# Kernel optimization log

Hardware: AMD Instinct MI355X
Metric: run time of the kernel (lower is better)

Reference implementation:

```python
import jax, jax.numpy as jnp
import numpy as np

B, S, P, HID, HQ, HKV, D, MAXP = 8, 4, 4096, 4096, 32, 8, 128, 8192


def setup_inputs() -> dict:
    key = jax.random.key(0)
    ks = jax.random.split(key, 8)
    # rotary tables (Llama-style: freqs duplicated across halves)
    inv_freq = 1.0 / (10000.0 ** (jnp.arange(0, D // 2, dtype=jnp.float32) / (D // 2)))
    t = jnp.arange(MAXP, dtype=jnp.float32)
    emb = jnp.concatenate([jnp.outer(t, inv_freq)] * 2, axis=-1)  # [MAXP, D]
    w = 0.02
    return {
        "x": jax.random.normal(ks[0], (B, S, HID), dtype=jnp.float32),
        "wq": w * jax.random.normal(ks[1], (HID, HQ * D), dtype=jnp.float32),
        "wk": w * jax.random.normal(ks[2], (HID, HKV * D), dtype=jnp.float32),
        "wv": w * jax.random.normal(ks[3], (HID, HKV * D), dtype=jnp.float32),
        "wo": w * jax.random.normal(ks[4], (HQ * D, HID), dtype=jnp.float32),
        "cos": jnp.cos(emb),
        "sin": jnp.sin(emb),
        "k_cache": jax.random.normal(ks[5], (B, P, HKV, D), dtype=jnp.float32),
        "v_cache": jax.random.normal(ks[6], (B, P, HKV, D), dtype=jnp.float32),
        "past_len": P,
    }


def _rope(x, c, s):
    # x: [B,S,H,D]; c,s: [1,S,1,D] -- half-rotation RoPE
    half = x.shape[-1] // 2
    x1, x2 = x[..., :half], x[..., half:]
    return x * c + jnp.concatenate([-x2, x1], axis=-1) * s


def reference(x, wq, wk, wv, wo, cos, sin, k_cache, v_cache, past_len):
    b, s, _ = x.shape
    hq, hkv, d = HQ, HKV, D
    q = (x @ wq).reshape(b, s, hq, d)
    k = (x @ wk).reshape(b, s, hkv, d)
    v = (x @ wv).reshape(b, s, hkv, d)

    pos = past_len + jnp.arange(s)                     # new-token positions
    c = cos[pos][None, :, None, :]
    sn = sin[pos][None, :, None, :]
    q = _rope(q, c, sn)
    k = _rope(k, c, sn)

    # append new kv to cache
    k_all = jnp.concatenate([k_cache, k], axis=1)      # [B,T,HKV,D]
    v_all = jnp.concatenate([v_cache, v], axis=1)
    t_len = k_all.shape[1]

    group = hq // hkv
    qg = q.reshape(b, s, hkv, group, d)
    scores = jnp.einsum('bskgd,btkd->bkgst', qg, k_all) / jnp.sqrt(jnp.asarray(d, x.dtype))

    # causal: query at position past_len+i attends to key positions <= past_len+i
    key_pos = jnp.arange(t_len)
    mask = pos[:, None] >= key_pos[None, :]            # [S,T]
    scores = jnp.where(mask[None, None, None], scores, jnp.asarray(-1e30, scores.dtype))
    attn = jax.nn.softmax(scores, axis=-1)

    out = jnp.einsum('bkgst,btkd->bskgd', attn, v_all).reshape(b, s, hq * d)
    return out @ wo
```

## Files before the change

kernel.cpp:

```cpp
#include <hip/hip_runtime.h>
#include <math.h>

#define NB 8
#define NS 4
#define NP 4096
#define HID 4096
#define NHQ 32
#define NHKV 8
#define ND 128
#define NGROUP 4
#define NBS 32
#define NQI 16
#define NCHUNK 17
#define TCHUNK 256
#define QKV_COLS 6144
#define LOG2E 1.4426950408889634f

__global__ __launch_bounds__(256) void prep_xT(const float* __restrict__ x,
                                               float* __restrict__ xT) {
  int n = blockIdx.x * 256 + threadIdx.x;
  int r = n >> 12;
  int k = n & 4095;
  xT[k * NBS + r] = x[n];
}

__global__ __launch_bounds__(256) void rope_kernel(
    const float* __restrict__ qb, const float* __restrict__ kb,
    const float* __restrict__ cosp, const float* __restrict__ sinp,
    const int* __restrict__ past_len, float* __restrict__ q_t,
    float* __restrict__ k_new) {
  int n = blockIdx.x * 256 + threadIdx.x;
  int pl = past_len[0];
  if (n < NBS * HID) {
    int r = n >> 12;
    int hd = n & 4095;
    int h = hd >> 7, d = hd & 127;
    int b = r >> 2, s = r & 3;
    int pos = pl + s;
    float c = cosp[pos * ND + d], sn = sinp[pos * ND + d];
    float v = qb[n];
    float other = (d < 64) ? -qb[n + 64] : qb[n - 64];
    float rv = fmaf(v, c, other * sn);
    int kv = h >> 2, g = h & 3;
    q_t[(((b * NHKV + kv) * ND + d) * NQI) + g * NS + s] = rv;
  } else {
    n -= NBS * HID;
    int r = n >> 10;
    int hd = n & 1023;
    int kv = hd >> 7, d = hd & 127;
    int b = r >> 2, s = r & 3;
    int pos = pl + s;
    float c = cosp[pos * ND + d], sn = sinp[pos * ND + d];
    float v = kb[n];
    float other = (d < 64) ? -kb[n + 64] : kb[n - 64];
    k_new[((b * NHKV + kv) * NS + s) * ND + d] = fmaf(v, c, other * sn);
  }
}

template <int KSLICE>
__global__ __launch_bounds__(256) void gemm_part(
    const float* __restrict__ A_T, const float* __restrict__ wq,
    const float* __restrict__ wk, const float* __restrict__ wv,
    const float* __restrict__ wo, float* __restrict__ P, int mode) {
  __shared__ __align__(16) float lds[8192];
  int cb = blockIdx.x, kb = blockIdx.y;
  int ncols = mode ? 4096 : QKV_COLS;
  int col0 = cb * 128;
  const float* W;
  int ld, wcol;
  if (mode) {
    W = wo; ld = 4096; wcol = col0;
  } else if (col0 < 4096) {
    W = wq; ld = 4096; wcol = col0;
  } else if (col0 < 5120) {
    W = wk; ld = 1024; wcol = col0 - 4096;
  } else {
    W = wv; ld = 1024; wcol = col0 - 5120;
  }
  int tid = threadIdx.x;
  int lane = tid & 63;
  int wid = __builtin_amdgcn_readfirstlane(tid >> 6);
  int l32 = lane & 31;
  int mh = lane >> 5;
  int kblk = kb * KSLICE;
  constexpr int KW = KSLICE / 4;
  int k0 = wid * KW;
  const float* wp = W + (size_t)(kblk + k0) * ld + wcol + l32 * 4;

  float4 wb[8];
#pragma unroll
  for (int u = 0; u < 8; u++) wb[u] = *(const float4*)(wp + (size_t)u * ld);

  {
    const float4* src = (const float4*)(A_T + (size_t)kblk * NBS);
    float4* dst = (float4*)lds;
#pragma unroll
    for (int p = 0; p < KSLICE / 32; p++)
      dst[p * 256 + tid] = src[p * 256 + tid];
  }
  __syncthreads();

  float acc[64];
#pragma unroll
  for (int v = 0; v < 64; v++) acc[v] = 0.f;

  const float* xp = lds + (size_t)k0 * NBS + mh * 16;

  auto body = [&](int kk, float4 w) {
    const float* xr = xp + (size_t)kk * NBS;
    float4 xa = *(const float4*)(xr);
    float4 xb = *(const float4*)(xr + 4);
    float4 xc = *(const float4*)(xr + 8);
    float4 xd = *(const float4*)(xr + 12);
    float xm[16] = {xa.x, xa.y, xa.z, xa.w, xb.x, xb.y, xb.z, xb.w,
                    xc.x, xc.y, xc.z, xc.w, xd.x, xd.y, xd.z, xd.w};
#pragma unroll
    for (int m = 0; m < 16; m++) {
      acc[4 * m + 0] = fmaf(xm[m], w.x, acc[4 * m + 0]);
      acc[4 * m + 1] = fmaf(xm[m], w.y, acc[4 * m + 1]);
      acc[4 * m + 2] = fmaf(xm[m], w.z, acc[4 * m + 2]);
      acc[4 * m + 3] = fmaf(xm[m], w.w, acc[4 * m + 3]);
    }
  };

#pragma unroll 8
  for (int kk = 0; kk < KW - 8; kk++) {
    float4 w = wb[kk & 7];
    wb[kk & 7] = *(const float4*)(wp + (size_t)(kk + 8) * ld);
    body(kk, w);
  }
#pragma unroll
  for (int kk = KW - 8; kk < KW; kk++) {
    float4 w = wb[kk & 7];
    body(kk, w);
  }

  __syncthreads();
  if (wid >= 2) {
#pragma unroll
    for (int v = 0; v < 64; v++) lds[(wid - 2) * 4096 + v * 64 + lane] = acc[v];
  }
  __syncthreads();
  if (wid < 2) {
#pragma unroll
    for (int v = 0; v < 64; v++) acc[v] += lds[wid * 4096 + v * 64 + lane];
  }
  __syncthreads();
  if (wid == 1) {
#pragma unroll
    for (int v = 0; v < 64; v++) lds[v * 64 + lane] = acc[v];
  }
  __syncthreads();
  if (wid == 0) {
#pragma unroll
    for (int v = 0; v < 64; v++) acc[v] += lds[v * 64 + lane];
#pragma unroll
    for (int m = 0; m < 16; m++) {
      float4 st = make_float4(acc[4 * m], acc[4 * m + 1], acc[4 * m + 2],
                              acc[4 * m + 3]);
      *(float4*)(P + ((size_t)kb * NBS + mh * 16 + m) * ncols + col0 +
                 l32 * 4) = st;
    }
  }
}

template <int KS>
__global__ __launch_bounds__(256) void reduce_qkv(const float* __restrict__ P,
                                                  float* __restrict__ qb,
                                                  float* __restrict__ kbuf,
                                                  float* __restrict__ vbuf) {
  size_t idx = ((size_t)blockIdx.x * 256 + threadIdx.x) * 4;
  float4 s = make_float4(0.f, 0.f, 0.f, 0.f);
#pragma unroll
  for (int p = 0; p < KS; p++) {
    float4 v = *(const float4*)(P + (size_t)p * (NBS * QKV_COLS) + idx);
    s.x += v.x; s.y += v.y; s.z += v.z; s.w += v.w;
  }
  int r = (int)(idx / QKV_COLS);
  int col = (int)(idx % QKV_COLS);
  float* dst;
  if (col < 4096)
    dst = qb + (size_t)r * 4096 + col;
  else if (col < 5120)
    dst = kbuf + (size_t)r * 1024 + (col - 4096);
  else
    dst = vbuf + (size_t)r * 1024 + (col - 5120);
  *(float4*)dst = s;
}

template <int KS>
__global__ __launch_bounds__(256) void reduce_o(const float* __restrict__ P,
                                                float* __restrict__ outp) {
  size_t idx = ((size_t)blockIdx.x * 256 + threadIdx.x) * 4;
  float4 s = make_float4(0.f, 0.f, 0.f, 0.f);
#pragma unroll
  for (int p = 0; p < KS; p++) {
    float4 v = *(const float4*)(P + (size_t)p * (NBS * 4096) + idx);
    s.x += v.x; s.y += v.y; s.z += v.z; s.w += v.w;
  }
  *(float4*)(outp + idx) = s;
}

__global__ __launch_bounds__(256) void attn_kernel(
    const float* __restrict__ q_t, const float* __restrict__ k_cache,
    const float* __restrict__ v_cache, const float* __restrict__ k_new,
    const float* __restrict__ vbuf, float* __restrict__ part_o,
    float* __restrict__ part_m, float* __restrict__ part_l) {
  __shared__ __align__(16) float sbuf[NQI * TCHUNK];
  __shared__ float redm[NQI][4];
  __shared__ float redl[NQI][4];
  __shared__ float mfin[NQI];
  float* p_lds = sbuf;
  int bk = blockIdx.x;
  int chunk = blockIdx.y;
  int blk = bk * NCHUNK + chunk;
  int b = bk >> 3, kv = bk & 7;
  int tid = threadIdx.x;
  int lane = tid & 63;
  int wid = tid >> 6;
  bool last = (chunk == NCHUNK - 1);
  int tcount = last ? NS : TCHUNK;
  const float* qbase = q_t + (size_t)bk * (ND * NQI);

  int t_loc = tid;
  bool valid = t_loc < tcount;
  int t_eff = valid ? t_loc : 0;
  const float* kp =
      last ? (k_new + ((size_t)bk * NS + t_eff) * ND)
           : (k_cache +
              (((size_t)b * NP + chunk * TCHUNK + t_eff) * NHKV + kv) * ND);
  float s_acc[NQI];
#pragma unroll
  for (int i = 0; i < NQI; i++) s_acc[i] = 0.f;
#pragma unroll 8
  for (int d4 = 0; d4 < 32; ++d4) {
    float4 kvv = *(const float4*)(kp + d4 * 4);
    const float* qp = qbase + (d4 * 4) * NQI;
#pragma unroll
    for (int i = 0; i < NQI; i++) {
      float s = s_acc[i];
      s = fmaf(kvv.x, qp[i], s);
      s = fmaf(kvv.y, qp[NQI + i], s);
      s = fmaf(kvv.z, qp[2 * NQI + i], s);
      s = fmaf(kvv.w, qp[3 * NQI + i], s);
      s_acc[i] = s;
    }
  }
  const float scale = 0.08838834764831845f;
  float sc[NQI];
#pragma unroll
  for (int i = 0; i < NQI; i++) {
    float s = s_acc[i] * scale;
    if (!valid || (last && t_loc > (i & 3))) s = -__builtin_inff();
    sc[i] = s;
  }
#pragma unroll
  for (int i = 0; i < NQI; i++) {
    float m = sc[i];
#pragma unroll
    for (int off = 1; off < 64; off <<= 1) m = fmaxf(m, __shfl_xor(m, off, 64));
    if (lane == 0) redm[i][wid] = m;
  }
  __syncthreads();
  if (tid < NQI) {
    mfin[tid] = fmaxf(fmaxf(redm[tid][0], redm[tid][1]),
                      fmaxf(redm[tid][2], redm[tid][3]));
  }
  __syncthreads();
  float l_loc[NQI];
#pragma unroll
  for (int i = 0; i < NQI; i++) {
    float p = exp2f((sc[i] - mfin[i]) * LOG2E);
    p_lds[i * TCHUNK + t_loc] = p;
    l_loc[i] = p;
  }
#pragma unroll
  for (int i = 0; i < NQI; i++) {
    float l = l_loc[i];
#pragma unroll
    for (int off = 1; off < 64; off <<= 1) l += __shfl_xor(l, off, 64);
    if (lane == 0) redl[i][wid] = l;
  }
  __syncthreads();
  if (tid < NQI) {
    part_m[(size_t)blk * NQI + tid] = mfin[tid];
    part_l[(size_t)blk * NQI + tid] =
        redl[tid][0] + redl[tid][1] + redl[tid][2] + redl[tid][3];
  }

  int g = tid >> 5;
  int dq = (tid & 31) * 4;
  int tbeg = g * 32;
  int tnum = tcount - tbeg;
  tnum = tnum < 0 ? 0 : (tnum > 32 ? 32 : tnum);
  const float* vpb =
      last ? (vbuf + ((size_t)b * NS + tbeg) * (NHKV * ND) + kv * ND + dq)
           : (v_cache + ((size_t)b * NP + chunk * TCHUNK + tbeg) * (NHKV * ND) +
              kv * ND + dq);
  float o[NQI][4];
#pragma unroll
  for (int i = 0; i < NQI; i++) o[i][0] = o[i][1] = o[i][2] = o[i][3] = 0.f;
#pragma unroll 4
  for (int tt = 0; tt < tnum; ++tt) {
    float4 vv = *(const float4*)(vpb + (size_t)tt * (NHKV * ND));
    const float* pp = p_lds + (tbeg + tt);
#pragma unroll
    for (int i = 0; i < NQI; i++) {
      float p = pp[i * TCHUNK];
      o[i][0] = fmaf(p, vv.x, o[i][0]);
      o[i][1] = fmaf(p, vv.y, o[i][1]);
      o[i][2] = fmaf(p, vv.z, o[i][2]);
      o[i][3] = fmaf(p, vv.w, o[i][3]);
    }
  }
#pragma unroll
  for (int i = 0; i < NQI; i++) {
#pragma unroll
    for (int c = 0; c < 4; c++) o[i][c] += __shfl_xor(o[i][c], 32, 64);
  }
  __syncthreads();
  float* red = sbuf;
  if (wid >= 2 && lane < 32) {
#pragma unroll
    for (int i = 0; i < NQI; i++)
      *(float4*)(red + ((wid - 2) * NQI + i) * 128 + dq) =
          make_float4(o[i][0], o[i][1], o[i][2], o[i][3]);
  }
  __syncthreads();
  if (wid < 2 && lane < 32) {
#pragma unroll
    for (int i = 0; i < NQI; i++) {
      float4 r = *(const float4*)(red + (wid * NQI + i) * 128 + dq);
      o[i][0] += r.x; o[i][1] += r.y; o[i][2] += r.z; o[i][3] += r.w;
    }
  }
  __syncthreads();
  if (wid == 1 && lane < 32) {
#pragma unroll
    for (int i = 0; i < NQI; i++)
      *(float4*)(red + i * 128 + dq) =
          make_float4(o[i][0], o[i][1], o[i][2], o[i][3]);
  }
  __syncthreads();
  if (wid == 0 && lane < 32) {
    size_t obase = (size_t)blk * (NQI * ND);
#pragma unroll
    for (int i = 0; i < NQI; i++) {
      float4 r = *(const float4*)(red + i * 128 + dq);
      *(float4*)(part_o + obase + (size_t)i * ND + dq) =
          make_float4(o[i][0] + r.x, o[i][1] + r.y, o[i][2] + r.z,
                      o[i][3] + r.w);
    }
  }
}

__global__ __launch_bounds__(256) void combine_kernel(
    const float* __restrict__ part_o, const float* __restrict__ part_m,
    const float* __restrict__ part_l, float* __restrict__ attn_T) {
  int bk = blockIdx.x;
  int tid = threadIdx.x;
  int i = tid >> 4;
  int dh = (tid & 15) * 4 + blockIdx.y * 64;
  float M = -__builtin_inff();
#pragma unroll
  for (int c = 0; c < NCHUNK; c++)
    M = fmaxf(M, part_m[((size_t)bk * NCHUNK + c) * NQI + i]);
  float L = 0.f;
  float o0 = 0.f, o1 = 0.f, o2 = 0.f, o3 = 0.f;
#pragma unroll
  for (int c = 0; c < NCHUNK; c++) {
    size_t pc = (size_t)bk * NCHUNK + c;
    float mc = part_m[pc * NQI + i];
    float w = exp2f((mc - M) * LOG2E);
    L = fmaf(part_l[pc * NQI + i], w, L);
    float4 po = *(const float4*)(part_o + pc * (NQI * ND) + (size_t)i * ND + dh);
    o0 = fmaf(w, po.x, o0);
    o1 = fmaf(w, po.y, o1);
    o2 = fmaf(w, po.z, o2);
    o3 = fmaf(w, po.w, o3);
  }
  float inv = 1.0f / L;
  int b = bk >> 3, kv = bk & 7;
  int g = i >> 2, s = i & 3;
  int h = kv * NGROUP + g;
  int r = b * NS + s;
  attn_T[(size_t)(h * ND + dh + 0) * NBS + r] = o0 * inv;
  attn_T[(size_t)(h * ND + dh + 1) * NBS + r] = o1 * inv;
  attn_T[(size_t)(h * ND + dh + 2) * NBS + r] = o2 * inv;
  attn_T[(size_t)(h * ND + dh + 3) * NBS + r] = o3 * inv;
}

extern "C" void kernel_launch(void* const* d_in, const int* in_sizes, int n_in,
                              void* d_out, int out_size, void* d_ws,
                              size_t ws_size, hipStream_t stream) {
  const float* x = (const float*)d_in[0];
  const float* wq = (const float*)d_in[1];
  const float* wk = (const float*)d_in[2];
  const float* wv = (const float*)d_in[3];
  const float* wo = (const float*)d_in[4];
  const float* cosp = (const float*)d_in[5];
  const float* sinp = (const float*)d_in[6];
  const float* k_cache = (const float*)d_in[7];
  const float* v_cache = (const float*)d_in[8];
  const int* past_len = (const int*)d_in[9];
  float* out = (float*)d_out;

  float* ws = (float*)d_ws;
  float* xT = ws;
  float* qb = xT + 131072;
  float* kbuf = qb + 131072;
  float* vbuf = kbuf + 32768;
  float* q_t = vbuf + 32768;
  float* k_new = q_t + 131072;
  float* attn_T = k_new + 32768;
  float* R = attn_T + 131072;
  float* Pq = R;
  float* part_o = R;
  float* part_m = R + 2228224;
  float* part_l = part_m + 17408;
  float* Po = R;

  const size_t need32 = (size_t)(622592 + 32 * NBS * QKV_COLS) * sizeof(float);
  const bool big = ws_size >= need32;

  prep_xT<<<512, 256, 0, stream>>>(x, xT);
  if (big) {
    gemm_part<128><<<dim3(48, 32), 256, 0, stream>>>(xT, wq, wk, wv, wo, Pq, 0);
    reduce_qkv<32><<<192, 256, 0, stream>>>(Pq, qb, kbuf, vbuf);
  } else {
    gemm_part<256><<<dim3(48, 16), 256, 0, stream>>>(xT, wq, wk, wv, wo, Pq, 0);
    reduce_qkv<16><<<192, 256, 0, stream>>>(Pq, qb, kbuf, vbuf);
  }
  rope_kernel<<<640, 256, 0, stream>>>(qb, kbuf, cosp, sinp, past_len, q_t,
                                       k_new);
  attn_kernel<<<dim3(64, NCHUNK), 256, 0, stream>>>(
      q_t, k_cache, v_cache, k_new, vbuf, part_o, part_m, part_l);
  combine_kernel<<<dim3(64, 2), 256, 0, stream>>>(part_o, part_m, part_l,
                                                  attn_T);
  if (big) {
    gemm_part<128><<<dim3(32, 32), 256, 0, stream>>>(attn_T, wq, wk, wv, wo,
                                                     Po, 1);
    reduce_o<32><<<128, 256, 0, stream>>>(Po, out);
  } else {
    gemm_part<256><<<dim3(32, 16), 256, 0, stream>>>(attn_T, wq, wk, wv, wo,
                                                     Po, 1);
    reduce_o<16><<<128, 256, 0, stream>>>(Po, out);
  }
}
```

Before: 464.6 us.

## Split attention into smaller chunks with head-dim split QK and query-half PV

The attention kernel is templated on chunk size. With enough workspace it uses 128-token chunks, giving 33 chunks and twice as many blocks. For those chunks the QK dot product is split across two thread halves over the head dimension and combined through LDS. The PV stage now gives each thread 8 queries instead of 16 and stores probabilities transposed with padding, which cuts register pressure and allows a higher occupancy hint. This adds more partials for the combine kernel, whose chunk loop is now a runtime count, and some extra LDS syncs.

```diff
diff --git a/kernel.cpp b/kernel.cpp
--- a/kernel.cpp
+++ b/kernel.cpp
@@ -11,8 +11,6 @@
 #define NGROUP 4
 #define NBS 32
 #define NQI 16
-#define NCHUNK 17
-#define TCHUNK 256
 #define QKV_COLS 6144
 #define LOG2E 1.4426950408889634f
 
@@ -201,153 +199,178 @@
   *(float4*)(outp + idx) = s;
 }
 
-__global__ __launch_bounds__(256) void attn_kernel(
+template <int TCH>
+__global__ __launch_bounds__(256, 6) void attn_kernel(
     const float* __restrict__ q_t, const float* __restrict__ k_cache,
     const float* __restrict__ v_cache, const float* __restrict__ k_new,
     const float* __restrict__ vbuf, float* __restrict__ part_o,
-    float* __restrict__ part_m, float* __restrict__ part_l) {
-  __shared__ __align__(16) float sbuf[NQI * TCHUNK];
+    float* __restrict__ part_m, float* __restrict__ part_l, int nch) {
+  constexpr int BUFN = (TCH * 17 > 4096) ? TCH * 17 : 4096;
+  constexpr int NWS = (TCH == 128) ? 2 : 4;
+  constexpr int NF4 = (TCH == 128) ? 16 : 32;
+  constexpr int TPV = TCH / 4;
+  __shared__ __align__(16) float sbuf[BUFN];
   __shared__ float redm[NQI][4];
   __shared__ float redl[NQI][4];
   __shared__ float mfin[NQI];
-  float* p_lds = sbuf;
   int bk = blockIdx.x;
   int chunk = blockIdx.y;
-  int blk = bk * NCHUNK + chunk;
+  int blk = bk * nch + chunk;
   int b = bk >> 3, kv = bk & 7;
   int tid = threadIdx.x;
   int lane = tid & 63;
   int wid = tid >> 6;
-  bool last = (chunk == NCHUNK - 1);
-  int tcount = last ? NS : TCHUNK;
+  bool last = (chunk == nch - 1);
+  int tcount = last ? NS : TCH;
   const float* qbase = q_t + (size_t)bk * (ND * NQI);
 
-  int t_loc = tid;
-  bool valid = t_loc < tcount;
-  int t_eff = valid ? t_loc : 0;
+  int t_loc = tid & (TCH - 1);
+  int dh = tid / TCH;
+  bool tvalid = t_loc < tcount;
+  int t_eff = tvalid ? t_loc : 0;
   const float* kp =
       last ? (k_new + ((size_t)bk * NS + t_eff) * ND)
            : (k_cache +
-              (((size_t)b * NP + chunk * TCHUNK + t_eff) * NHKV + kv) * ND);
+              (((size_t)b * NP + chunk * TCH + t_eff) * NHKV + kv) * ND);
+  kp += dh * 64;
   float s_acc[NQI];
 #pragma unroll
   for (int i = 0; i < NQI; i++) s_acc[i] = 0.f;
-#pragma unroll 8
-  for (int d4 = 0; d4 < 32; ++d4) {
-    float4 kvv = *(const float4*)(kp + d4 * 4);
-    const float* qp = qbase + (d4 * 4) * NQI;
-#pragma unroll
-    for (int i = 0; i < NQI; i++) {
-      float s = s_acc[i];
-      s = fmaf(kvv.x, qp[i], s);
-      s = fmaf(kvv.y, qp[NQI + i], s);
-      s = fmaf(kvv.z, qp[2 * NQI + i], s);
-      s = fmaf(kvv.w, qp[3 * NQI + i], s);
-      s_acc[i] = s;
+#pragma unroll 4
+  for (int i = 0; i < NF4; ++i) {
+    float4 kvv = *(const float4*)(kp + i * 4);
+    const float* qp = qbase + (dh * 64 + i * 4) * NQI;
+#pragma unroll
+    for (int q = 0; q < NQI; q++) {
+      float s = s_acc[q];
+      s = fmaf(kvv.x, qp[q], s);
+      s = fmaf(kvv.y, qp[NQI + q], s);
+      s = fmaf(kvv.z, qp[2 * NQI + q], s);
+      s = fmaf(kvv.w, qp[3 * NQI + q], s);
+      s_acc[q] = s;
+    }
+  }
+  if (TCH == 128) {
+    if (dh == 1) {
+#pragma unroll
+      for (int q = 0; q < NQI; q++) sbuf[t_loc * 17 + q] = s_acc[q];
+    }
+    __syncthreads();
+    if (dh == 0) {
+#pragma unroll
+      for (int q = 0; q < NQI; q++) s_acc[q] += sbuf[t_loc * 17 + q];
     }
   }
   const float scale = 0.08838834764831845f;
   float sc[NQI];
 #pragma unroll
-  for (int i = 0; i < NQI; i++) {
-    float s = s_acc[i] * scale;
-    if (!valid || (last && t_loc > (i & 3))) s = -__builtin_inff();
-    sc[i] = s;
-  }
-#pragma unroll
-  for (int i = 0; i < NQI; i++) {
-    float m = sc[i];
+  for (int q = 0; q < NQI; q++) {
+    float s = s_acc[q] * scale;
+    if (dh != 0 || !tvalid || (last && t_loc > (q & 3)))
+      s = -__builtin_inff();
+    sc[q] = s;
+  }
+#pragma unroll
+  for (int q = 0; q < NQI; q++) {
+    float m = sc[q];
 #pragma unroll
     for (int off = 1; off < 64; off <<= 1) m = fmaxf(m, __shfl_xor(m, off, 64));
-    if (lane == 0) redm[i][wid] = m;
+    if (lane == 0 && wid < NWS) redm[q][wid] = m;
   }
   __syncthreads();
   if (tid < NQI) {
-    mfin[tid] = fmaxf(fmaxf(redm[tid][0], redm[tid][1]),
-                      fmaxf(redm[tid][2], redm[tid][3]));
+    float m = redm[tid][0];
+#pragma unroll
+    for (int w = 1; w < NWS; w++) m = fmaxf(m, redm[tid][w]);
+    mfin[tid] = m;
   }
   __syncthreads();
   float l_loc[NQI];
-#pragma unroll
-  for (int i = 0; i < NQI; i++) {
-    float p = exp2f((sc[i] - mfin[i]) * LOG2E);
-    p_lds[i * TCHUNK + t_loc] = p;
-    l_loc[i] = p;
-  }
-#pragma unroll
-  for (int i = 0; i < NQI; i++) {
-    float l = l_loc[i];
-#pragma unroll
-    for (int off = 1; off < 64; off <<= 1) l += __shfl_xor(l, off, 64);
-    if (lane == 0) redl[i][wid] = l;
+  if (dh == 0) {
+#pragma unroll
+    for (int q = 0; q < NQI; q++) {
+      float p = exp2f((sc[q] - mfin[q]) * LOG2E);
+      sbuf[t_loc * 17 + q] = p;
+      l_loc[q] = p;
+    }
+  } else {
+#pragma unroll
+    for (int q = 0; q < NQI; q++) l_loc[q] = 0.f;
+  }
+  if (wid < NWS) {
+#pragma unroll
+    for (int q = 0; q < NQI; q++) {
+      float l = l_loc[q];
+#pragma unroll
+      for (int off = 1; off < 64; off <<= 1) l += __shfl_xor(l, off, 64);
+      if (lane == 0) redl[q][wid] = l;
+    }
   }
   __syncthreads();
   if (tid < NQI) {
+    float l = redl[tid][0];
+#pragma unroll
+    for (int w = 1; w < NWS; w++) l += redl[tid][w];
     part_m[(size_t)blk * NQI + tid] = mfin[tid];
-    part_l[(size_t)blk * NQI + tid] =
-        redl[tid][0] + redl[tid][1] + redl[tid][2] + redl[tid][3];
+    part_l[(size_t)blk * NQI + tid] = l;
   }
 
   int g = tid >> 5;
+  int qh = g & 1;
+  int tq = g >> 1;
   int dq = (tid & 31) * 4;
-  int tbeg = g * 32;
+  int tbeg = tq * TPV;
   int tnum = tcount - tbeg;
-  tnum = tnum < 0 ? 0 : (tnum > 32 ? 32 : tnum);
+  tnum = tnum < 0 ? 0 : (tnum > TPV ? TPV : tnum);
   const float* vpb =
       last ? (vbuf + ((size_t)b * NS + tbeg) * (NHKV * ND) + kv * ND + dq)
-           : (v_cache + ((size_t)b * NP + chunk * TCHUNK + tbeg) * (NHKV * ND) +
+           : (v_cache + ((size_t)b * NP + chunk * TCH + tbeg) * (NHKV * ND) +
               kv * ND + dq);
-  float o[NQI][4];
-#pragma unroll
-  for (int i = 0; i < NQI; i++) o[i][0] = o[i][1] = o[i][2] = o[i][3] = 0.f;
+  float o[8][4];
+#pragma unroll
+  for (int i = 0; i < 8; i++) o[i][0] = o[i][1] = o[i][2] = o[i][3] = 0.f;
 #pragma unroll 4
   for (int tt = 0; tt < tnum; ++tt) {
     float4 vv = *(const float4*)(vpb + (size_t)tt * (NHKV * ND));
-    const float* pp = p_lds + (tbeg + tt);
-#pragma unroll
-    for (int i = 0; i < NQI; i++) {
-      float p = pp[i * TCHUNK];
+    const float* pp = sbuf + (tbeg + tt) * 17 + qh * 8;
+#pragma unroll
+    for (int i = 0; i < 8; i++) {
+      float p = pp[i];
       o[i][0] = fmaf(p, vv.x, o[i][0]);
       o[i][1] = fmaf(p, vv.y, o[i][1]);
       o[i][2] = fmaf(p, vv.z, o[i][2]);
       o[i][3] = fmaf(p, vv.w, o[i][3]);
     }
   }
-#pragma unroll
-  for (int i = 0; i < NQI; i++) {
-#pragma unroll
-    for (int c = 0; c < 4; c++) o[i][c] += __shfl_xor(o[i][c], 32, 64);
-  }
-  __syncthreads();
-  float* red = sbuf;
-  if (wid >= 2 && lane < 32) {
-#pragma unroll
-    for (int i = 0; i < NQI; i++)
-      *(float4*)(red + ((wid - 2) * NQI + i) * 128 + dq) =
+  __syncthreads();
+  if (wid >= 2) {
+#pragma unroll
+    for (int i = 0; i < 8; i++)
+      *(float4*)(sbuf + (wid - 2) * 2048 + i * 256 + lane * 4) =
           make_float4(o[i][0], o[i][1], o[i][2], o[i][3]);
   }
   __syncthreads();
-  if (wid < 2 && lane < 32) {
-#pragma unroll
-    for (int i = 0; i < NQI; i++) {
-      float4 r = *(const float4*)(red + (wid * NQI + i) * 128 + dq);
+  if (wid < 2) {
+#pragma unroll
+    for (int i = 0; i < 8; i++) {
+      float4 r = *(const float4*)(sbuf + wid * 2048 + i * 256 + lane * 4);
       o[i][0] += r.x; o[i][1] += r.y; o[i][2] += r.z; o[i][3] += r.w;
     }
   }
   __syncthreads();
-  if (wid == 1 && lane < 32) {
-#pragma unroll
-    for (int i = 0; i < NQI; i++)
-      *(float4*)(red + i * 128 + dq) =
+  if (wid == 1) {
+#pragma unroll
+    for (int i = 0; i < 8; i++)
+      *(float4*)(sbuf + i * 256 + lane * 4) =
           make_float4(o[i][0], o[i][1], o[i][2], o[i][3]);
   }
   __syncthreads();
-  if (wid == 0 && lane < 32) {
+  if (wid == 0) {
     size_t obase = (size_t)blk * (NQI * ND);
 #pragma unroll
-    for (int i = 0; i < NQI; i++) {
-      float4 r = *(const float4*)(red + i * 128 + dq);
-      *(float4*)(part_o + obase + (size_t)i * ND + dq) =
+    for (int i = 0; i < 8; i++) {
+      float4 r = *(const float4*)(sbuf + i * 256 + lane * 4);
+      *(float4*)(part_o + obase + (size_t)(qh * 8 + i) * ND + dq) =
           make_float4(o[i][0] + r.x, o[i][1] + r.y, o[i][2] + r.z,
                       o[i][3] + r.w);
     }
@@ -356,20 +379,18 @@
 
 __global__ __launch_bounds__(256) void combine_kernel(
     const float* __restrict__ part_o, const float* __restrict__ part_m,
-    const float* __restrict__ part_l, float* __restrict__ attn_T) {
+    const float* __restrict__ part_l, float* __restrict__ attn_T, int nch) {
   int bk = blockIdx.x;
   int tid = threadIdx.x;
   int i = tid >> 4;
   int dh = (tid & 15) * 4 + blockIdx.y * 64;
   float M = -__builtin_inff();
-#pragma unroll
-  for (int c = 0; c < NCHUNK; c++)
-    M = fmaxf(M, part_m[((size_t)bk * NCHUNK + c) * NQI + i]);
+  for (int c = 0; c < nch; c++)
+    M = fmaxf(M, part_m[((size_t)bk * nch + c) * NQI + i]);
   float L = 0.f;
   float o0 = 0.f, o1 = 0.f, o2 = 0.f, o3 = 0.f;
-#pragma unroll
-  for (int c = 0; c < NCHUNK; c++) {
-    size_t pc = (size_t)bk * NCHUNK + c;
+  for (int c = 0; c < nch; c++) {
+    size_t pc = (size_t)bk * nch + c;
     float mc = part_m[pc * NQI + i];
     float w = exp2f((mc - M) * LOG2E);
     L = fmaf(part_l[pc * NQI + i], w, L);
@@ -414,17 +435,24 @@
   float* k_new = q_t + 131072;
   float* attn_T = k_new + 32768;
   float* R = attn_T + 131072;
+
+  size_t ws_fl = ws_size / sizeof(float);
+  int ksplit, nch;
+  if (ws_fl >= (size_t)622592 + 6291456) {
+    ksplit = 32; nch = 33;
+  } else if (ws_fl >= (size_t)622592 + 4392960) {
+    ksplit = 16; nch = 33;
+  } else {
+    ksplit = 16; nch = 17;
+  }
   float* Pq = R;
   float* part_o = R;
-  float* part_m = R + 2228224;
-  float* part_l = part_m + 17408;
+  float* part_m = R + (size_t)64 * nch * 2048;
+  float* part_l = part_m + (size_t)64 * nch * 16;
   float* Po = R;
 
-  const size_t need32 = (size_t)(622592 + 32 * NBS * QKV_COLS) * sizeof(float);
-  const bool big = ws_size >= need32;
-
   prep_xT<<<512, 256, 0, stream>>>(x, xT);
-  if (big) {
+  if (ksplit == 32) {
     gemm_part<128><<<dim3(48, 32), 256, 0, stream>>>(xT, wq, wk, wv, wo, Pq, 0);
     reduce_qkv<32><<<192, 256, 0, stream>>>(Pq, qb, kbuf, vbuf);
   } else {
@@ -433,11 +461,16 @@
   }
   rope_kernel<<<640, 256, 0, stream>>>(qb, kbuf, cosp, sinp, past_len, q_t,
                                        k_new);
-  attn_kernel<<<dim3(64, NCHUNK), 256, 0, stream>>>(
-      q_t, k_cache, v_cache, k_new, vbuf, part_o, part_m, part_l);
+  if (nch == 33) {
+    attn_kernel<128><<<dim3(64, 33), 256, 0, stream>>>(
+        q_t, k_cache, v_cache, k_new, vbuf, part_o, part_m, part_l, 33);
+  } else {
+    attn_kernel<256><<<dim3(64, 17), 256, 0, stream>>>(
+        q_t, k_cache, v_cache, k_new, vbuf, part_o, part_m, part_l, 17);
+  }
   combine_kernel<<<dim3(64, 2), 256, 0, stream>>>(part_o, part_m, part_l,
-                                                  attn_T);
-  if (big) {
+                                                  attn_T, nch);
+  if (ksplit == 32) {
     gemm_part<128><<<dim3(32, 32), 256, 0, stream>>>(attn_T, wq, wk, wv, wo,
                                                      Po, 1);
     reduce_o<32><<<128, 256, 0, stream>>>(Po, out);
```

After: 506.2 us. +9.0%, slower.
